# Optimization experiments

Hardware: AMD Instinct MI355X
Metric: run time of the kernel (lower is better)

Reference implementation:

```python
import jax, jax.numpy as jnp
import numpy as np

BATCH, SEQ, D_IN, H = 16, 1024, 128, 64


def setup_inputs() -> dict:
    key = jax.random.key(0)
    k1, k2, k3, k4 = jax.random.split(key, 4)
    x = jax.random.normal(k1, (BATCH, SEQ, D_IN), dtype=jnp.float32)
    B = jax.random.normal(k2, (H, D_IN), dtype=jnp.float32)
    nu = jax.random.normal(k3, (H,), dtype=jnp.float32)
    theta = jax.random.normal(k4, (H,), dtype=jnp.float32)
    return {"x": x, "B": B, "nu": nu, "theta": theta}


def reference(x, B, nu, theta):
    # x: [b, t, j]; B: [h, j]; nu, theta: [h]
    T = x.shape[1]
    lam = jnp.exp(-jnp.exp(nu) + 1j * theta)  # [h] complex64
    Bx = jnp.einsum('hj,btj->bth', B, x).astype(jnp.complex64)  # [b, t, h]
    # lam^|s - t| for all pairs, upper triangle only (s <= t)
    idx = jnp.arange(T)
    time_diffs = jnp.abs(idx[:, None] - idx[None, :])  # [s, t]
    lam_powers = jnp.triu(lam[:, None, None] ** time_diffs)  # [h, s, t]
    out = jnp.einsum('hst,bsh->bth', lam_powers, Bx)  # [b, t, h] complex
    # initial-state contribution: h0 = ones(b, h)
    h0 = jnp.ones((x.shape[0], lam.shape[0]), dtype=jnp.complex64)
    out = out + (lam[None, :, None].transpose(0, 2, 1) ** jnp.arange(1, T + 1, dtype=jnp.float32)[None, :, None]) * h0[:, None, :]
    return jnp.concatenate([out.real.astype(jnp.float32), out.imag.astype(jnp.float32)], axis=2)
```

## Files before the change

kernel.cpp:

```cpp
#include <hip/hip_runtime.h>
#include <math.h>

#define NB 16
#define T_SEQ 1024
#define DIN 128
#define NH 64

__global__ __launch_bounds__(256) void k_gemm(const float* __restrict__ x,
                                              const float* __restrict__ Bm,
                                              float* __restrict__ bx) {
    __shared__ float sB[NH * DIN];
    const int tid = threadIdx.x;
    for (int i = tid; i < NH * DIN / 4; i += 256)
        reinterpret_cast<float4*>(sB)[i] = reinterpret_cast<const float4*>(Bm)[i];
    __syncthreads();

    const int wave = tid >> 6, lane = tid & 63;
    const int row = blockIdx.x * 64 + lane;
    const int b = row >> 10, t = row & 1023;
    const float* xr = x + (size_t)row * DIN;

    float acc[16];
#pragma unroll
    for (int i = 0; i < 16; ++i) acc[i] = 0.f;

    for (int jc = 0; jc < DIN / 4; ++jc) {
        const float4 xv = reinterpret_cast<const float4*>(xr)[jc];
#pragma unroll
        for (int hh = 0; hh < 16; ++hh) {
            const int h = wave * 16 + hh;
            const float4 bv = reinterpret_cast<const float4*>(sB + h * DIN)[jc];
            acc[hh] += xv.x * bv.x + xv.y * bv.y + xv.z * bv.z + xv.w * bv.w;
        }
    }
#pragma unroll
    for (int hh = 0; hh < 16; ++hh) {
        const int h = wave * 16 + hh;
        bx[((size_t)(b * NH + h) << 10) + t] = acc[hh];
    }
}

__global__ __launch_bounds__(256) void k_scan(const float* __restrict__ nu,
                                              const float* __restrict__ theta,
                                              float* __restrict__ R,
                                              float* __restrict__ I) {
    const int wave = threadIdx.x >> 6, lane = threadIdx.x & 63;
    const int wid = blockIdx.x * 4 + wave;
    const int h = wid & (NH - 1);

    const float env = expf(nu[h]);
    const float th = theta[h];

    float s1, c1; sincosf(th, &s1, &c1);
    const float mag1 = expf(-env);
    const float lr = mag1 * c1, li = mag1 * s1;

    float* rowR = R + ((size_t)wid << 10);
    float* rowI = I + ((size_t)wid << 10);

    float pr[16], pi[16];
#pragma unroll
    for (int q = 0; q < 4; ++q) {
        const float4 u4 = reinterpret_cast<const float4*>(rowR + lane * 16)[q];
        pr[q * 4 + 0] = u4.x; pr[q * 4 + 1] = u4.y;
        pr[q * 4 + 2] = u4.z; pr[q * 4 + 3] = u4.w;
    }

    float sr = 0.f, si = 0.f;
#pragma unroll
    for (int i = 0; i < 16; ++i) {
        const float u = pr[i];
        const float nr = lr * sr - li * si + u;
        const float ni = lr * si + li * sr;
        pr[i] = nr; pi[i] = ni;
        sr = nr; si = ni;
    }

    float fs_, fc_; sincosf(16.f * th, &fs_, &fc_);
    const float fmag = expf(-16.f * env);
    float dr = fmag * fc_, di = fmag * fs_;
    float vr = sr, vi = si;
#pragma unroll
    for (int d = 1; d < 64; d <<= 1) {
        const float orr = __shfl_up(vr, d, 64);
        const float oii = __shfl_up(vi, d, 64);
        if (lane >= d) {
            vr += dr * orr - di * oii;
            vi += dr * oii + di * orr;
        }
        const float t2r = dr * dr - di * di;
        const float t2i = 2.f * dr * di;
        dr = t2r; di = t2i;
    }

    float cr = __shfl_up(vr, 1, 64);
    float ci = __shfl_up(vi, 1, 64);
    if (lane == 0) { cr = 0.f; ci = 0.f; }
    float gs_, gc_; sincosf(16.f * (float)lane * th, &gs_, &gc_);
    const float gmag = expf(-16.f * (float)lane * env);
    const float gr = cr + gmag * gc_;
    const float gi = ci + gmag * gs_;

    float lpr = lr, lpi = li;
#pragma unroll
    for (int i = 0; i < 16; ++i) {
        const float hr = lpr * gr - lpi * gi + pr[i];
        const float hi = lpr * gi + lpi * gr + pi[i];
        pr[i] = hr; pi[i] = hi;
        const float nr = lpr * lr - lpi * li;
        const float ni = lpr * li + lpi * lr;
        lpr = nr; lpi = ni;
    }

#pragma unroll
    for (int q = 0; q < 4; ++q) {
        float4 o;
        o.x = pr[q * 4 + 0]; o.y = pr[q * 4 + 1];
        o.z = pr[q * 4 + 2]; o.w = pr[q * 4 + 3];
        reinterpret_cast<float4*>(rowR + lane * 16)[q] = o;
        float4 oi;
        oi.x = pi[q * 4 + 0]; oi.y = pi[q * 4 + 1];
        oi.z = pi[q * 4 + 2]; oi.w = pi[q * 4 + 3];
        reinterpret_cast<float4*>(rowI + lane * 16)[q] = oi;
    }
}

__global__ __launch_bounds__(256) void k_tr(const float* __restrict__ R,
                                            const float* __restrict__ I,
                                            float* __restrict__ out) {
    __shared__ float s[64][129];
    const int b = blockIdx.x >> 4;
    const int t0 = (blockIdx.x & 15) * 64;
    const int tid = threadIdx.x;

#pragma unroll
    for (int k = 0; k < 4; ++k) {
        const int q = tid + k * 256;
        const int hh = q >> 4, t4 = q & 15;
        const float4 v = reinterpret_cast<const float4*>(
            R + (((size_t)(b * NH + hh) << 10) + t0))[t4];
        s[t4 * 4 + 0][hh] = v.x; s[t4 * 4 + 1][hh] = v.y;
        s[t4 * 4 + 2][hh] = v.z; s[t4 * 4 + 3][hh] = v.w;
    }
#pragma unroll
    for (int k = 0; k < 4; ++k) {
        const int q = tid + k * 256;
        const int hh = q >> 4, t4 = q & 15;
        const float4 v = reinterpret_cast<const float4*>(
            I + (((size_t)(b * NH + hh) << 10) + t0))[t4];
        s[t4 * 4 + 0][64 + hh] = v.x; s[t4 * 4 + 1][64 + hh] = v.y;
        s[t4 * 4 + 2][64 + hh] = v.z; s[t4 * 4 + 3][64 + hh] = v.w;
    }
    __syncthreads();

    const size_t obase = ((size_t)b * T_SEQ + t0) * 128;
#pragma unroll
    for (int k = 0; k < 32; ++k) {
        const int q = tid + k * 256;
        out[obase + q] = s[q >> 7][q & 127];
    }
}

extern "C" void kernel_launch(void* const* d_in, const int* in_sizes, int n_in,
                              void* d_out, int out_size, void* d_ws, size_t ws_size,
                              hipStream_t stream) {
    const float* x  = (const float*)d_in[0];
    const float* Bm = (const float*)d_in[1];
    const float* nu = (const float*)d_in[2];
    const float* th = (const float*)d_in[3];
    float* out = (float*)d_out;

    float* R = (float*)d_ws;
    float* I = R + (1 << 20);

    k_gemm<<<256, 256, 0, stream>>>(x, Bm, R);
    k_scan<<<256, 256, 0, stream>>>(nu, th, R, I);
    k_tr  <<<256, 256, 0, stream>>>(R, I, out);
}
```

Baseline: 87.16 us.

## Fuse scan with transpose via LDS and read B directly from global

The scan and transpose kernels are merged into one 1024-thread kernel per (batch, 16-head group). Scan results are staged in swizzled LDS and written out as float4 in the final [b,t,2h] layout, so the intermediate real/imag buffers no longer round-trip through global memory and one launch is removed. The GEMM drops its shared-memory staging of B and loads B rows through wave-uniform (readfirstlane) addresses, with explicit FMA chains and a partial unroll. The trade-off is only 64 blocks for the fused kernel, which may underfill the GPU, and B reads now depend on cache behaviour.

```diff
diff --git a/kernel.cpp b/kernel.cpp
--- a/kernel.cpp
+++ b/kernel.cpp
@@ -1,7 +1,6 @@
 #include <hip/hip_runtime.h>
 #include <math.h>
 
-#define NB 16
 #define T_SEQ 1024
 #define DIN 128
 #define NH 64
@@ -9,61 +8,62 @@
 __global__ __launch_bounds__(256) void k_gemm(const float* __restrict__ x,
                                               const float* __restrict__ Bm,
                                               float* __restrict__ bx) {
-    __shared__ float sB[NH * DIN];
     const int tid = threadIdx.x;
-    for (int i = tid; i < NH * DIN / 4; i += 256)
-        reinterpret_cast<float4*>(sB)[i] = reinterpret_cast<const float4*>(Bm)[i];
-    __syncthreads();
-
-    const int wave = tid >> 6, lane = tid & 63;
+    const int wave = __builtin_amdgcn_readfirstlane(tid >> 6);
+    const int lane = tid & 63;
     const int row = blockIdx.x * 64 + lane;
     const int b = row >> 10, t = row & 1023;
-    const float* xr = x + (size_t)row * DIN;
+    const float4* xr = reinterpret_cast<const float4*>(x + (size_t)row * DIN);
+    const float4* Br = reinterpret_cast<const float4*>(Bm + (size_t)wave * 16 * DIN);
 
     float acc[16];
 #pragma unroll
     for (int i = 0; i < 16; ++i) acc[i] = 0.f;
 
+#pragma unroll 2
     for (int jc = 0; jc < DIN / 4; ++jc) {
-        const float4 xv = reinterpret_cast<const float4*>(xr)[jc];
+        const float4 xv = xr[jc];
 #pragma unroll
         for (int hh = 0; hh < 16; ++hh) {
-            const int h = wave * 16 + hh;
-            const float4 bv = reinterpret_cast<const float4*>(sB + h * DIN)[jc];
-            acc[hh] += xv.x * bv.x + xv.y * bv.y + xv.z * bv.z + xv.w * bv.w;
+            const float4 bv = Br[hh * 32 + jc];
+            acc[hh] = fmaf(xv.x, bv.x,
+                      fmaf(xv.y, bv.y,
+                      fmaf(xv.z, bv.z,
+                      fmaf(xv.w, bv.w, acc[hh]))));
         }
     }
 #pragma unroll
-    for (int hh = 0; hh < 16; ++hh) {
-        const int h = wave * 16 + hh;
-        bx[((size_t)(b * NH + h) << 10) + t] = acc[hh];
-    }
+    for (int hh = 0; hh < 16; ++hh)
+        bx[((size_t)((b << 6) + (wave << 4) + hh) << 10) + t] = acc[hh];
 }
 
-__global__ __launch_bounds__(256) void k_scan(const float* __restrict__ nu,
-                                              const float* __restrict__ theta,
-                                              float* __restrict__ R,
-                                              float* __restrict__ I) {
-    const int wave = threadIdx.x >> 6, lane = threadIdx.x & 63;
-    const int wid = blockIdx.x * 4 + wave;
-    const int h = wid & (NH - 1);
+__global__ __launch_bounds__(1024) void k_scan_tr(const float* __restrict__ nu,
+                                                  const float* __restrict__ theta,
+                                                  const float* __restrict__ R,
+                                                  float* __restrict__ out) {
+    __shared__ float sR[16][1028];
+    __shared__ float sI[16][1028];
+    const int tid = threadIdx.x;
+    const int w = __builtin_amdgcn_readfirstlane(tid >> 6);
+    const int lane = tid & 63;
+    const int b = blockIdx.x >> 2;
+    const int hg = blockIdx.x & 3;
+    const int h = hg * 16 + w;
+    const int wid = (b << 6) + h;
 
     const float env = expf(nu[h]);
     const float th = theta[h];
-
     float s1, c1; sincosf(th, &s1, &c1);
     const float mag1 = expf(-env);
     const float lr = mag1 * c1, li = mag1 * s1;
 
-    float* rowR = R + ((size_t)wid << 10);
-    float* rowI = I + ((size_t)wid << 10);
-
+    const float4* rowR = reinterpret_cast<const float4*>(R + ((size_t)wid << 10));
     float pr[16], pi[16];
 #pragma unroll
     for (int q = 0; q < 4; ++q) {
-        const float4 u4 = reinterpret_cast<const float4*>(rowR + lane * 16)[q];
-        pr[q * 4 + 0] = u4.x; pr[q * 4 + 1] = u4.y;
-        pr[q * 4 + 2] = u4.z; pr[q * 4 + 3] = u4.w;
+        const float4 u4 = rowR[lane * 4 + q];
+        pr[4 * q + 0] = u4.x; pr[4 * q + 1] = u4.y;
+        pr[4 * q + 2] = u4.z; pr[4 * q + 3] = u4.w;
     }
 
     float sr = 0.f, si = 0.f;
@@ -114,50 +114,31 @@
 
 #pragma unroll
     for (int q = 0; q < 4; ++q) {
-        float4 o;
-        o.x = pr[q * 4 + 0]; o.y = pr[q * 4 + 1];
-        o.z = pr[q * 4 + 2]; o.w = pr[q * 4 + 3];
-        reinterpret_cast<float4*>(rowR + lane * 16)[q] = o;
-        float4 oi;
-        oi.x = pi[q * 4 + 0]; oi.y = pi[q * 4 + 1];
-        oi.z = pi[q * 4 + 2]; oi.w = pi[q * 4 + 3];
-        reinterpret_cast<float4*>(rowI + lane * 16)[q] = oi;
-    }
-}
-
-__global__ __launch_bounds__(256) void k_tr(const float* __restrict__ R,
-                                            const float* __restrict__ I,
-                                            float* __restrict__ out) {
-    __shared__ float s[64][129];
-    const int b = blockIdx.x >> 4;
-    const int t0 = (blockIdx.x & 15) * 64;
-    const int tid = threadIdx.x;
-
-#pragma unroll
-    for (int k = 0; k < 4; ++k) {
-        const int q = tid + k * 256;
-        const int hh = q >> 4, t4 = q & 15;
-        const float4 v = reinterpret_cast<const float4*>(
-            R + (((size_t)(b * NH + hh) << 10) + t0))[t4];
-        s[t4 * 4 + 0][hh] = v.x; s[t4 * 4 + 1][hh] = v.y;
-        s[t4 * 4 + 2][hh] = v.z; s[t4 * 4 + 3][hh] = v.w;
-    }
-#pragma unroll
-    for (int k = 0; k < 4; ++k) {
-        const int q = tid + k * 256;
-        const int hh = q >> 4, t4 = q & 15;
-        const float4 v = reinterpret_cast<const float4*>(
-            I + (((size_t)(b * NH + hh) << 10) + t0))[t4];
-        s[t4 * 4 + 0][64 + hh] = v.x; s[t4 * 4 + 1][64 + hh] = v.y;
-        s[t4 * 4 + 2][64 + hh] = v.z; s[t4 * 4 + 3][64 + hh] = v.w;
+        const int pos = 16 * lane + 4 * ((q + lane) & 3);
+        *reinterpret_cast<float4*>(&sR[w][pos]) =
+            make_float4(pr[4 * q + 0], pr[4 * q + 1], pr[4 * q + 2], pr[4 * q + 3]);
+        *reinterpret_cast<float4*>(&sI[w][pos]) =
+            make_float4(pi[4 * q + 0], pi[4 * q + 1], pi[4 * q + 2], pi[4 * q + 3]);
     }
     __syncthreads();
 
-    const size_t obase = ((size_t)b * T_SEQ + t0) * 128;
+    const size_t ob = (size_t)b * (T_SEQ * 128) + hg * 16;
 #pragma unroll
-    for (int k = 0; k < 32; ++k) {
-        const int q = tid + k * 256;
-        out[obase + q] = s[q >> 7][q & 127];
+    for (int k = 0; k < 8; ++k) {
+        const int part = k >> 2;
+        const int f2 = tid + (k & 3) * 1024;
+        const int c = f2 & 3;
+        const int t = f2 >> 2;
+        const int pos = (t & ~15) | ((((t >> 2) + (t >> 4)) & 3) << 2) | (t & 3);
+        float4 v;
+        if (part == 0) {
+            v.x = sR[4 * c + 0][pos]; v.y = sR[4 * c + 1][pos];
+            v.z = sR[4 * c + 2][pos]; v.w = sR[4 * c + 3][pos];
+        } else {
+            v.x = sI[4 * c + 0][pos]; v.y = sI[4 * c + 1][pos];
+            v.z = sI[4 * c + 2][pos]; v.w = sI[4 * c + 3][pos];
+        }
+        *reinterpret_cast<float4*>(&out[ob + (size_t)t * 128 + part * 64 + 4 * c]) = v;
     }
 }
 
@@ -171,9 +152,7 @@
     float* out = (float*)d_out;
 
     float* R = (float*)d_ws;
-    float* I = R + (1 << 20);
 
-    k_gemm<<<256, 256, 0, stream>>>(x, Bm, R);
-    k_scan<<<256, 256, 0, stream>>>(nu, th, R, I);
-    k_tr  <<<256, 256, 0, stream>>>(R, I, out);
+    k_gemm   <<<256, 256, 0, stream>>>(x, Bm, R);
+    k_scan_tr<<< 64, 1024, 0, stream>>>(nu, th, R, out);
 }
```

Result: slower. 92.10 us (+5.7%).
